# Optimization experiments

Hardware: AMD Instinct MI355X
Metric: run time of the kernel (lower is better)

Reference implementation:

```python
import jax, jax.numpy as jnp
import numpy as np

B, S, DK = 32, 2048, 64

def setup_inputs() -> dict:
    key = jax.random.key(0)
    kq, kk, kv = jax.random.split(key, 3)
    Q = jax.random.normal(kq, (B, S, DK), dtype=jnp.float32)
    K = jax.random.normal(kk, (B, S, DK), dtype=jnp.float32)
    V = jax.random.normal(kv, (B, S, DK), dtype=jnp.float32)
    return {"Q": Q, "K": K, "V": V}

def reference(Q, K, V):
    # attn_scores = Q K^T / sqrt(d_k); full [B,S,S] probs materialized (naive, non-flash)
    d_k = Q.shape[-1]
    scores = jnp.einsum('bqd,bkd->bqk', Q, K) / jnp.sqrt(jnp.asarray(d_k, Q.dtype))
    probs = jax.nn.softmax(scores, axis=-1)
    return jnp.einsum('bqk,bkd->bqd', probs, V)
```

## Files before the change

### kernel.cpp

```cpp
#include <hip/hip_runtime.h>

#define BATCH 32
#define SEQ   2048
#define DKK   64

constexpr int QT = 128;
constexpr int KT = 64;
constexpr int NW = 8;
constexpr int WQ = 16;

typedef __attribute__((ext_vector_type(8))) short bf16x8;
typedef __attribute__((ext_vector_type(4))) float f32x4;
typedef __attribute__((ext_vector_type(4))) short short4v;

__device__ __forceinline__ short f2bf(float f) {
    union { float f; unsigned u; } c; c.f = f;
    unsigned r = c.u + 0x7fffu + ((c.u >> 16) & 1u);
    return (short)(r >> 16);
}

__device__ __forceinline__ float fast_exp2(float x) {
#if __has_builtin(__builtin_amdgcn_exp2f)
    return __builtin_amdgcn_exp2f(x);
#else
    return exp2f(x);
#endif
}

__global__ __launch_bounds__(512, 4) void attn_fwd(
        const float* __restrict__ Q, const float* __restrict__ K,
        const float* __restrict__ V, float* __restrict__ O) {
    __shared__ short Kb[KT][DKK + 8];
    __shared__ short Vt[DKK][KT + 8];
    __shared__ short Pb[NW][WQ][KT + 8];

    const int tid  = threadIdx.x;
    const int w    = tid >> 6;
    const int lane = tid & 63;
    const int quad = lane >> 4;
    const int l15  = lane & 15;
    const int b    = blockIdx.y;
    const int q0   = blockIdx.x * QT + w * WQ;

    const float qscale = 0.125f * 1.44269504088896340736f;
    bf16x8 qfrag[2];
    #pragma unroll
    for (int ks = 0; ks < 2; ++ks) {
        const float* qp = Q + ((size_t)b * SEQ + q0 + l15) * DKK + 32*ks + quad*8;
        float4 a = *(const float4*)qp;
        float4 c = *(const float4*)(qp + 4);
        bf16x8 f;
        f[0]=f2bf(a.x*qscale); f[1]=f2bf(a.y*qscale); f[2]=f2bf(a.z*qscale); f[3]=f2bf(a.w*qscale);
        f[4]=f2bf(c.x*qscale); f[5]=f2bf(c.y*qscale); f[6]=f2bf(c.z*qscale); f[7]=f2bf(c.w*qscale);
        qfrag[ks] = f;
    }

    f32x4 o[4] = {};
    float lsum[4] = {};

    const float* Kbase = K + (size_t)b * SEQ * DKK;
    const float* Vbase = V + (size_t)b * SEQ * DKK;

    for (int kb = 0; kb < SEQ; kb += KT) {
        __syncthreads();
        {
            const float* Kg = Kbase + (size_t)kb * DKK;
            #pragma unroll
            for (int i = 0; i < 2; ++i) {
                int f   = tid + 512*i;
                int row = f >> 4;
                int c4  = (f & 15) << 2;
                float4 kv = *(const float4*)(Kg + row*DKK + c4);
                short4v kk;
                kk[0]=f2bf(kv.x); kk[1]=f2bf(kv.y); kk[2]=f2bf(kv.z); kk[3]=f2bf(kv.w);
                *(short4v*)&Kb[row][c4] = kk;
            }
            const float* Vg = Vbase + (size_t)(kb + w*8) * DKK + lane;
            #pragma unroll
            for (int c = 0; c < 2; ++c) {
                short4v t;
                #pragma unroll
                for (int i = 0; i < 4; ++i) t[i] = f2bf(Vg[(4*c + i) * DKK]);
                *(short4v*)&Vt[lane][w*8 + 4*c] = t;
            }
        }
        __syncthreads();

        f32x4 sc[4];
        #pragma unroll
        for (int nt = 0; nt < 4; ++nt) {
            bf16x8 kf0 = *(const bf16x8*)&Kb[16*nt + l15][quad*8];
            bf16x8 kf1 = *(const bf16x8*)&Kb[16*nt + l15][32 + quad*8];
            f32x4 acc = {};
            acc = __builtin_amdgcn_mfma_f32_16x16x32_bf16(qfrag[0], kf0, acc, 0, 0, 0);
            acc = __builtin_amdgcn_mfma_f32_16x16x32_bf16(qfrag[1], kf1, acc, 0, 0, 0);
            sc[nt] = acc;
        }

        #pragma unroll
        for (int nt = 0; nt < 4; ++nt)
            #pragma unroll
            for (int j = 0; j < 4; ++j) {
                float p = fast_exp2(sc[nt][j]);
                lsum[j] += p;
                Pb[w][4*quad + j][16*nt + l15] = f2bf(p);
            }

        #pragma unroll
        for (int ks = 0; ks < 2; ++ks) {
            bf16x8 pa = *(const bf16x8*)&Pb[w][l15][32*ks + quad*8];
            #pragma unroll
            for (int nt = 0; nt < 4; ++nt) {
                bf16x8 vf = *(const bf16x8*)&Vt[16*nt + l15][32*ks + quad*8];
                o[nt] = __builtin_amdgcn_mfma_f32_16x16x32_bf16(pa, vf, o[nt], 0, 0, 0);
            }
        }
    }

    #pragma unroll
    for (int j = 0; j < 4; ++j) {
        float s = lsum[j];
        s += __shfl_xor(s, 1);
        s += __shfl_xor(s, 2);
        s += __shfl_xor(s, 4);
        s += __shfl_xor(s, 8);
        lsum[j] = 1.0f / s;
    }

    #pragma unroll
    for (int j = 0; j < 4; ++j) {
        float inv = lsum[j];
        float* op = O + ((size_t)b * SEQ + q0 + 4*quad + j) * DKK + l15;
        #pragma unroll
        for (int nt = 0; nt < 4; ++nt)
            op[16*nt] = o[nt][j] * inv;
    }
}

extern "C" void kernel_launch(void* const* d_in, const int* in_sizes, int n_in,
                              void* d_out, int out_size, void* d_ws, size_t ws_size,
                              hipStream_t stream) {
    const float* Q = (const float*)d_in[0];
    const float* K = (const float*)d_in[1];
    const float* V = (const float*)d_in[2];
    float* O = (float*)d_out;
    dim3 grid(SEQ / QT, BATCH);
    attn_fwd<<<grid, dim3(512), 0, stream>>>(Q, K, V, O);
}
```

Baseline: 151.9 us.

## Transpose MFMA operand order so each lane owns one query row

Swaps the A/B operands of both MFMAs so the score and output accumulators are transposed, giving each lane a single query row with four contiguous key/dim elements. This lets P be written to shared memory as packed 8-byte stores instead of scalar shorts, cuts the row-sum reduction to one scalar with two shuffles, and makes output writes float4-vectorized. The V transpose load is also remapped. It aims to reduce LDS store count, shuffle work and scattered global stores, at the risk of changing LDS bank-conflict patterns.

After: 151.2 us. Within noise of the previous version (-0.4%).

```diff
diff --git a/kernel.cpp b/kernel.cpp
--- a/kernel.cpp
+++ b/kernel.cpp
@@ -19,6 +19,10 @@
     return (short)(r >> 16);
 }
 
+__device__ __forceinline__ unsigned pack2(short lo, short hi) {
+    return (unsigned)(unsigned short)lo | ((unsigned)(unsigned short)hi << 16);
+}
+
 __device__ __forceinline__ float fast_exp2(float x) {
 #if __has_builtin(__builtin_amdgcn_exp2f)
     return __builtin_amdgcn_exp2f(x);
@@ -30,10 +34,9 @@
 __global__ __launch_bounds__(512, 4) void attn_fwd(
         const float* __restrict__ Q, const float* __restrict__ K,
         const float* __restrict__ V, float* __restrict__ O) {
-    __shared__ short Kb[KT][DKK + 8];
-    __shared__ short Vt[DKK][KT + 8];
-    __shared__ short Pb[NW][WQ][KT + 8];
-
+    __shared__ short Kb[KT][72];
+    __shared__ short Vt[DKK][72];
+    __shared__ short Pb[NW][WQ][72];
     const int tid  = threadIdx.x;
     const int w    = tid >> 6;
     const int lane = tid & 63;
@@ -56,10 +59,12 @@
     }
 
     f32x4 o[4] = {};
-    float lsum[4] = {};
+    float lsum = 0.f;
 
     const float* Kbase = K + (size_t)b * SEQ * DKK;
     const float* Vbase = V + (size_t)b * SEQ * DKK;
+
+    const int kg = (w & 3) * 16 + 4 * quad;
 
     for (int kb = 0; kb < SEQ; kb += KT) {
         __syncthreads();
@@ -75,65 +80,67 @@
                 kk[0]=f2bf(kv.x); kk[1]=f2bf(kv.y); kk[2]=f2bf(kv.z); kk[3]=f2bf(kv.w);
                 *(short4v*)&Kb[row][c4] = kk;
             }
-            const float* Vg = Vbase + (size_t)(kb + w*8) * DKK + lane;
             #pragma unroll
-            for (int c = 0; c < 2; ++c) {
+            for (int cc = 0; cc < 2; ++cc) {
+                int d = l15 + 16 * (2*(w>>2) + cc);
+                const float* Vp = Vbase + (size_t)(kb + kg) * DKK + d;
                 short4v t;
                 #pragma unroll
-                for (int i = 0; i < 4; ++i) t[i] = f2bf(Vg[(4*c + i) * DKK]);
-                *(short4v*)&Vt[lane][w*8 + 4*c] = t;
+                for (int i = 0; i < 4; ++i) t[i] = f2bf(Vp[i*DKK]);
+                *(short4v*)&Vt[d][kg] = t;
             }
         }
         __syncthreads();
 
         f32x4 sc[4];
         #pragma unroll
-        for (int nt = 0; nt < 4; ++nt) {
-            bf16x8 kf0 = *(const bf16x8*)&Kb[16*nt + l15][quad*8];
-            bf16x8 kf1 = *(const bf16x8*)&Kb[16*nt + l15][32 + quad*8];
+        for (int kt = 0; kt < 4; ++kt) {
+            bf16x8 kf0 = *(const bf16x8*)&Kb[16*kt + l15][quad*8];
+            bf16x8 kf1 = *(const bf16x8*)&Kb[16*kt + l15][32 + quad*8];
             f32x4 acc = {};
-            acc = __builtin_amdgcn_mfma_f32_16x16x32_bf16(qfrag[0], kf0, acc, 0, 0, 0);
-            acc = __builtin_amdgcn_mfma_f32_16x16x32_bf16(qfrag[1], kf1, acc, 0, 0, 0);
-            sc[nt] = acc;
+            acc = __builtin_amdgcn_mfma_f32_16x16x32_bf16(kf0, qfrag[0], acc, 0, 0, 0);
+            acc = __builtin_amdgcn_mfma_f32_16x16x32_bf16(kf1, qfrag[1], acc, 0, 0, 0);
+            sc[kt] = acc;
         }
 
         #pragma unroll
-        for (int nt = 0; nt < 4; ++nt)
-            #pragma unroll
-            for (int j = 0; j < 4; ++j) {
-                float p = fast_exp2(sc[nt][j]);
-                lsum[j] += p;
-                Pb[w][4*quad + j][16*nt + l15] = f2bf(p);
-            }
+        for (int kt = 0; kt < 4; ++kt) {
+            float p0 = fast_exp2(sc[kt][0]);
+            float p1 = fast_exp2(sc[kt][1]);
+            float p2 = fast_exp2(sc[kt][2]);
+            float p3 = fast_exp2(sc[kt][3]);
+            lsum += (p0 + p1) + (p2 + p3);
+            int2 pw;
+            pw.x = (int)pack2(f2bf(p0), f2bf(p1));
+            pw.y = (int)pack2(f2bf(p2), f2bf(p3));
+            *(int2*)&Pb[w][l15][16*kt + 4*quad] = pw;
+        }
 
         #pragma unroll
         for (int ks = 0; ks < 2; ++ks) {
-            bf16x8 pa = *(const bf16x8*)&Pb[w][l15][32*ks + quad*8];
+            bf16x8 pf = *(const bf16x8*)&Pb[w][l15][32*ks + quad*8];
             #pragma unroll
             for (int nt = 0; nt < 4; ++nt) {
                 bf16x8 vf = *(const bf16x8*)&Vt[16*nt + l15][32*ks + quad*8];
-                o[nt] = __builtin_amdgcn_mfma_f32_16x16x32_bf16(pa, vf, o[nt], 0, 0, 0);
+                o[nt] = __builtin_amdgcn_mfma_f32_16x16x32_bf16(vf, pf, o[nt], 0, 0, 0);
             }
         }
     }
 
+    float s = lsum;
+    s += __shfl_xor(s, 16);
+    s += __shfl_xor(s, 32);
+    const float inv = 1.0f / s;
+
+    float* op = O + ((size_t)b * SEQ + q0 + l15) * DKK + 4*quad;
     #pragma unroll
-    for (int j = 0; j < 4; ++j) {
-        float s = lsum[j];
-        s += __shfl_xor(s, 1);
-        s += __shfl_xor(s, 2);
-        s += __shfl_xor(s, 4);
-        s += __shfl_xor(s, 8);
-        lsum[j] = 1.0f / s;
-    }
-
-    #pragma unroll
-    for (int j = 0; j < 4; ++j) {
-        float inv = lsum[j];
-        float* op = O + ((size_t)b * SEQ + q0 + 4*quad + j) * DKK + l15;
-        #pragma unroll
-        for (int nt = 0; nt < 4; ++nt)
-            op[16*nt] = o[nt][j] * inv;
+    for (int nt = 0; nt < 4; ++nt) {
+        float4 st;
+        st.x = o[nt][0] * inv;
+        st.y = o[nt][1] * inv;
+        st.z = o[nt][2] * inv;
+        st.w = o[nt][3] * inv;
+        *(float4*)(op + 16*nt) = st;
     }
 }
 
```
